# Kernel optimization log

Hardware: AMD Instinct MI355X
Metric: run time of the kernel (lower is better)

Reference implementation:

```python
import jax, jax.numpy as jnp
import numpy as np

N_NODES = 100000
N_EDGES = 3200000
F_IN = 128
F_HID = 16
F_OUT = 1


def setup_inputs() -> dict:
    key = jax.random.key(0)
    ks = jax.random.split(key, 8)
    x = jax.random.normal(ks[0], (N_NODES, F_IN), dtype=jnp.float32)
    src = jax.random.randint(ks[1], (N_EDGES,), 0, N_NODES, dtype=jnp.int32)
    dst = jax.random.randint(ks[2], (N_EDGES,), 0, N_NODES, dtype=jnp.int32)
    edge_w = jax.random.uniform(ks[3], (N_EDGES,), dtype=jnp.float32)
    W0 = jax.random.normal(ks[4], (F_IN, F_HID), dtype=jnp.float32) / np.sqrt(F_IN)
    b0 = jnp.zeros((F_HID,), dtype=jnp.float32)
    W1 = jax.random.normal(ks[5], (F_HID, F_OUT), dtype=jnp.float32) / np.sqrt(F_HID)
    b1 = jnp.zeros((F_OUT,), dtype=jnp.float32)
    return {"x": x, "src": src, "dst": dst, "edge_w": edge_w,
            "W0": W0, "b0": b0, "W1": W1, "b1": b1}


def _spmm(src, dst, edge_w, h):
    # sparse A (COO) @ dense h: gather rows at src, weight, scatter-add to dst
    msgs = h[src] * edge_w[:, None]            # [E, F]
    return jax.ops.segment_sum(msgs, dst, num_segments=N_NODES)  # [N, F]


def reference(x, src, dst, edge_w, W0, b0, W1, b1):
    # GCNConv layer 0: relu(A @ (x @ W0) + b0)
    z0 = x @ W0                                 # [N, 16] linear transform first
    h = jax.nn.relu(_spmm(src, dst, edge_w, z0) + b0)
    # (Dropout is identity at inference)
    # GCNConv layer 1: sigmoid(A @ (h @ W1) + b1)
    z1 = h @ W1                                 # [N, 1]
    out = jax.nn.sigmoid(_spmm(src, dst, edge_w, z1) + b1)
    return out
```

## Files before the change

### kernel.cpp

```cpp
#include <hip/hip_runtime.h>

#define N_NODES 100000
#define N_EDGES 3200000
#define F_IN 128
#define F_HID 16

#define BK_LG 9
#define BK_NODES 512
#define NBK ((N_NODES + BK_NODES - 1) / BK_NODES)
#define NBK_P 256
#define BCAP 17664
#define CH1 2048
#define NCH1 ((N_EDGES + CH1 - 1) / CH1)
#define CUR_STRIDE 16

__device__ __forceinline__ unsigned short f2bf_rne(float f) {
    unsigned u = __float_as_uint(f);
    u += 0x7FFFu + ((u >> 16) & 1u);
    return (unsigned short)(u >> 16);
}

__global__ __launch_bounds__(256) void k_pre(const float* __restrict__ x,
                                             const float* __restrict__ W0,
                                             unsigned short* __restrict__ z0b,
                                             const int* __restrict__ src,
                                             const int* __restrict__ dst,
                                             const float* __restrict__ ew,
                                             int* __restrict__ cursorC,
                                             int2* __restrict__ ebinC) {
    __shared__ __align__(16) char smem[24832];
    const int tid = threadIdx.x;

    if ((blockIdx.x & 1) == 0) {
        const int xb = blockIdx.x >> 1;
        unsigned short* xsb = (unsigned short*)smem;
        float* w0s = (float*)(smem + 16640);
        for (int i = tid; i < F_IN * F_HID; i += 256) w0s[i] = W0[i];
        const int row0 = xb * 64;
        for (int i = tid; i < 64 * 32; i += 256) {
            int r = i >> 5, c4 = i & 31;
            float4 v = make_float4(0.f, 0.f, 0.f, 0.f);
            int row = row0 + r;
            if (row < N_NODES) v = ((const float4*)(x + (size_t)row * F_IN))[c4];
            *(ushort2*)(xsb + r * 130 + c4 * 4)     = make_ushort2(f2bf_rne(v.x), f2bf_rne(v.y));
            *(ushort2*)(xsb + r * 130 + c4 * 4 + 2) = make_ushort2(f2bf_rne(v.z), f2bf_rne(v.w));
        }
        __syncthreads();
        const int r  = tid & 63;
        const int cg = tid >> 6;
        float a0 = 0.f, a1 = 0.f, a2 = 0.f, a3 = 0.f;
        #pragma unroll 4
        for (int k = 0; k < F_IN; k += 2) {
            unsigned u = *(const unsigned*)(xsb + r * 130 + k);
            float xv0 = __uint_as_float(u << 16);
            float xv1 = __uint_as_float(u & 0xFFFF0000u);
            const float* wr0 = w0s + k * F_HID + cg * 4;
            const float* wr1 = wr0 + F_HID;
            a0 = fmaf(xv0, wr0[0], a0); a1 = fmaf(xv0, wr0[1], a1);
            a2 = fmaf(xv0, wr0[2], a2); a3 = fmaf(xv0, wr0[3], a3);
            a0 = fmaf(xv1, wr1[0], a0); a1 = fmaf(xv1, wr1[1], a1);
            a2 = fmaf(xv1, wr1[2], a2); a3 = fmaf(xv1, wr1[3], a3);
        }
        int row = row0 + r;
        if (row < N_NODES) {
            ushort4 p = make_ushort4(f2bf_rne(a0), f2bf_rne(a1),
                                     f2bf_rne(a2), f2bf_rne(a3));
            *(ushort4*)(z0b + (size_t)row * F_HID + cg * 4) = p;
        }
    } else {
        const int ch = blockIdx.x >> 1;
        int2* stage = (int2*)smem;
        unsigned char* sbid = (unsigned char*)(smem + 16384);
        int* cnt  = (int*)(smem + 18432);
        int* excl = (int*)(smem + 19456);
        int* run  = (int*)(smem + 20480);
        int* gb   = (int*)(smem + 21504);
        int* alw  = (int*)(smem + 22528);
        int* wtot = (int*)(smem + 23552);
        const int e0  = ch * CH1;
        const int nch = min(CH1, N_EDGES - e0);

        cnt[tid] = 0;
        __syncthreads();

        int es[8], eb[8], edl[8]; float ww[8];
        #pragma unroll
        for (int k = 0; k < 8; ++k) {
            int idx = k * 256 + tid;
            if (idx < nch) {
                int e = e0 + idx;
                int d = dst[e];
                es[k]  = src[e];
                ww[k]  = ew[e];
                eb[k]  = d >> BK_LG;
                edl[k] = d & (BK_NODES - 1);
                atomicAdd(&cnt[eb[k]], 1);
            } else {
                eb[k] = -1;
            }
        }
        __syncthreads();

        {
            const int lane = tid & 63, wid = tid >> 6;
            int c_ = cnt[tid], inc = c_;
            #pragma unroll
            for (int off = 1; off < 64; off <<= 1) {
                int t = __shfl_up(inc, off);
                if (lane >= off) inc += t;
            }
            if (lane == 63) wtot[wid] = inc;
            __syncthreads();
            int base = 0;
            #pragma unroll
            for (int w = 0; w < 4; ++w) base += (w < wid) ? wtot[w] : 0;
            excl[tid] = base + inc - c_;
        }
        __syncthreads();

        if (tid < NBK) {
            int c = cnt[tid];
            if (c > 0) {
                int old = atomicAdd(&cursorC[tid * CUR_STRIDE], c);
                int a = BCAP - old;
                a = (a < 0) ? 0 : ((a > c) ? c : a);
                alw[tid] = a;
                gb[tid]  = tid * BCAP + old;
            } else {
                alw[tid] = 0;
                gb[tid]  = tid * BCAP;
            }
            run[tid] = 0;
        }
        __syncthreads();

        #pragma unroll
        for (int k = 0; k < 8; ++k) {
            if (eb[k] >= 0) {
                int b = eb[k];
                int p = excl[b] + atomicAdd(&run[b], 1);
                stage[p] = make_int2(__float_as_int(ww[k]), es[k] | (edl[k] << 17));
                sbid[p]  = (unsigned char)b;
            }
        }
        __syncthreads();

        for (int s = tid; s < nch; s += 256) {
            int b   = sbid[s];
            int off = s - excl[b];
            if (off < alw[b]) ebinC[(size_t)gb[b] + off] = stage[s];
        }
    }
}

__global__ __launch_bounds__(512) void k_sort2(const int* __restrict__ cursorC,
                                               const int2* __restrict__ ebinC,
                                               int2* __restrict__ sortedC,
                                               int2* __restrict__ rowinfo) {
    __shared__ int dcnt[BK_NODES], excl[BK_NODES], run[BK_NODES];
    __shared__ int wtot[8];
    const int tid = threadIdx.x, lane = tid & 63, wid = tid >> 6;
    const int c = blockIdx.x;
    dcnt[tid] = 0; run[tid] = 0;
    __syncthreads();
    const int   ecnt = min(cursorC[c * CUR_STRIDE], BCAP);
    const int2* eC   = ebinC + (size_t)c * BCAP;
    for (int i = tid; i < ecnt; i += 512) atomicAdd(&dcnt[eC[i].y >> 17], 1);
    __syncthreads();
    int d_ = dcnt[tid], inc = d_;
    #pragma unroll
    for (int off = 1; off < 64; off <<= 1) {
        int t = __shfl_up(inc, off);
        if (lane >= off) inc += t;
    }
    if (lane == 63) wtot[wid] = inc;
    __syncthreads();
    int base = 0;
    #pragma unroll
    for (int w = 0; w < 8; ++w) base += (w < wid) ? wtot[w] : 0;
    int ex = base + inc - d_;
    excl[tid] = ex;
    int v = c * BK_NODES + tid;
    if (v < N_NODES) rowinfo[v] = make_int2(c * BCAP + ex, d_);
    __syncthreads();
    int2* oB = sortedC + (size_t)c * BCAP;
    for (int i = tid; i < ecnt; i += 512) {
        int2 e = eC[i];
        int dl = e.y >> 17;
        int p  = excl[dl] + atomicAdd(&run[dl], 1);
        oB[p] = e;
    }
}

__global__ __launch_bounds__(256) void k_g0(const int2* __restrict__ rowinfo,
                                            const int2* __restrict__ sortedC,
                                            const unsigned short* __restrict__ z0b,
                                            const float* __restrict__ b0,
                                            const float* __restrict__ W1,
                                            float* __restrict__ z1) {
    __shared__ float b0s[16], w1s[16];
    const int tid = threadIdx.x;
    if (tid < 16) { b0s[tid] = b0[tid]; w1s[tid] = W1[tid]; }
    __syncthreads();
    const int lane = tid & 63;
    const int v    = blockIdx.x * 4 + (tid >> 6);
    if (v >= N_NODES) return;
    const int2 ri  = rowinfo[v];
    const int2* sl = sortedC + ri.x;
    const int dv   = ri.y;
    const int f2   = lane & 7;
    const int g    = lane >> 3;
    float acc0 = 0.f, acc1 = 0.f;
    for (int j = g; j < dv; j += 16) {
        int2 e0 = sl[j];
        int  j1 = j + 8;
        int2 e1 = (j1 < dv) ? sl[j1] : make_int2(0, 0);
        unsigned u0 = *(const unsigned*)(z0b + (size_t)(e0.y & 0x1FFFF) * F_HID + f2 * 2);
        unsigned u1 = *(const unsigned*)(z0b + (size_t)(e1.y & 0x1FFFF) * F_HID + f2 * 2);
        float w0 = __int_as_float(e0.x), w1 = __int_as_float(e1.x);
        acc0 = fmaf(__uint_as_float(u0 << 16),         w0, acc0);
        acc1 = fmaf(__uint_as_float(u0 & 0xFFFF0000u), w0, acc1);
        acc0 = fmaf(__uint_as_float(u1 << 16),         w1, acc0);
        acc1 = fmaf(__uint_as_float(u1 & 0xFFFF0000u), w1, acc1);
    }
    acc0 += __shfl_xor(acc0, 8);  acc1 += __shfl_xor(acc1, 8);
    acc0 += __shfl_xor(acc0, 16); acc1 += __shfl_xor(acc1, 16);
    acc0 += __shfl_xor(acc0, 32); acc1 += __shfl_xor(acc1, 32);
    float cc = fmaxf(acc0 + b0s[f2 * 2], 0.f) * w1s[f2 * 2]
             + fmaxf(acc1 + b0s[f2 * 2 + 1], 0.f) * w1s[f2 * 2 + 1];
    cc += __shfl_xor(cc, 1);
    cc += __shfl_xor(cc, 2);
    cc += __shfl_xor(cc, 4);
    if (lane == 0) z1[v] = cc;
}

__global__ __launch_bounds__(256) void k_g1(const int2* __restrict__ rowinfo,
                                            const int2* __restrict__ sortedC,
                                            const float* __restrict__ z1,
                                            const float* __restrict__ b1,
                                            float* __restrict__ out) {
    const int tid = threadIdx.x;
    const int l8  = tid & 7;
    const int v   = blockIdx.x * 32 + (tid >> 3);
    if (v >= N_NODES) return;
    const int2 ri  = rowinfo[v];
    const int2* sl = sortedC + ri.x;
    const int dv   = ri.y;
    float acc = 0.f;
    for (int j = l8; j < dv; j += 16) {
        int2 e0 = sl[j];
        int  j1 = j + 8;
        int2 e1 = (j1 < dv) ? sl[j1] : make_int2(0, 0);
        acc = fmaf(z1[e0.y & 0x1FFFF], __int_as_float(e0.x), acc);
        acc = fmaf(z1[e1.y & 0x1FFFF], __int_as_float(e1.x), acc);
    }
    #pragma unroll
    for (int off = 1; off < 8; off <<= 1) acc += __shfl_xor(acc, off);
    if (l8 == 0) {
        float t = acc + b1[0];
        out[v] = 1.f / (1.f + expf(-t));
    }
}

extern "C" void kernel_launch(void* const* d_in, const int* in_sizes, int n_in,
                              void* d_out, int out_size, void* d_ws, size_t ws_size,
                              hipStream_t stream) {
    const float* x   = (const float*)d_in[0];
    const int*   src = (const int*)d_in[1];
    const int*   dst = (const int*)d_in[2];
    const float* ew  = (const float*)d_in[3];
    const float* W0  = (const float*)d_in[4];
    const float* b0  = (const float*)d_in[5];
    const float* W1  = (const float*)d_in[6];
    const float* b1  = (const float*)d_in[7];
    float* out = (float*)d_out;

    unsigned short* z0b = (unsigned short*)d_ws;
    float* z1      = (float*)(z0b + (size_t)N_NODES * F_HID);
    int*   cursorC = (int*)(z1 + N_NODES);
    int2*  rowinfo = (int2*)(cursorC + NBK * CUR_STRIDE);
    int2*  ebinC   = rowinfo + N_NODES;
    int2*  sortedC = ebinC + (size_t)NBK * BCAP;

    hipMemsetAsync(cursorC, 0, (size_t)NBK * CUR_STRIDE * sizeof(int), stream);

    k_pre  <<<2 * NCH1, 256, 0, stream>>>(x, W0, z0b, src, dst, ew, cursorC, ebinC);
    k_sort2<<<NBK, 512, 0, stream>>>(cursorC, ebinC, sortedC, rowinfo);
    k_g0   <<<(N_NODES + 3) / 4,   256, 0, stream>>>(rowinfo, sortedC, z0b, b0, W1, z1);
    k_g1   <<<(N_NODES + 31) / 32, 256, 0, stream>>>(rowinfo, sortedC, z1, b1, out);
}
```

Baseline: 151.4 us.

## Restructure binning into coarse buckets and fuse fine sort with layer-0 gather

Edge binning now uses coarse 1024-node buckets in larger 4096-edge chunks, with per-wave histograms to cut shared atomic contention. A new fused kernel has each 128-node fine bucket scan its coarse slab, counting-sort its edges in LDS, write the sorted list for layer 1, and run the layer-0 gather directly from LDS. The x@W0 projection is split back into its own kernel, and the memset becomes a tiny kernel. The cost is that each coarse slab is read eight times, and there is less overlap between projection and binning.

```diff
diff --git a/kernel.cpp b/kernel.cpp
--- a/kernel.cpp
+++ b/kernel.cpp
@@ -5,13 +5,18 @@
 #define F_IN 128
 #define F_HID 16
 
-#define BK_LG 9
-#define BK_NODES 512
-#define NBK ((N_NODES + BK_NODES - 1) / BK_NODES)
-#define NBK_P 256
-#define BCAP 17664
-#define CH1 2048
-#define NCH1 ((N_EDGES + CH1 - 1) / CH1)
+#define BK_LG 7
+#define BK_NODES 128
+#define NB ((N_NODES + BK_NODES - 1) / BK_NODES)
+#define BCAPF 4736
+#define CLG 10
+#define CNODES 1024
+#define NBC ((N_NODES + CNODES - 1) / CNODES)
+#define NBC_P 128
+#define BCAPC 34816
+#define CHUNK1 4096
+#define NCH1 ((N_EDGES + CHUNK1 - 1) / CHUNK1)
+#define NXB ((N_NODES + 63) / 64)
 #define CUR_STRIDE 16
 
 __device__ __forceinline__ unsigned short f2bf_rne(float f) {
@@ -20,222 +25,258 @@
     return (unsigned short)(u >> 16);
 }
 
-__global__ __launch_bounds__(256) void k_pre(const float* __restrict__ x,
+__global__ __launch_bounds__(256) void k_zc(int* __restrict__ cursorC) {
+    int i = blockIdx.x * 256 + threadIdx.x;
+    if (i < NBC * CUR_STRIDE) cursorC[i] = 0;
+}
+
+__global__ __launch_bounds__(512) void k_bin1(const int* __restrict__ src,
+                                              const int* __restrict__ dst,
+                                              const float* __restrict__ ew,
+                                              int* __restrict__ cursorC,
+                                              int2* __restrict__ ebinC) {
+    __shared__ int2 stage[CHUNK1];
+    __shared__ unsigned char sbid[CHUNK1];
+    __shared__ int cntw[8 * NBC_P];
+    __shared__ int runw[8 * NBC_P];
+    __shared__ int basew[8 * NBC_P];
+    __shared__ int cnt[NBC_P], excl[NBC_P], gb[NBC_P], alw[NBC_P];
+    __shared__ int wtot[2];
+    const int tid  = threadIdx.x;
+    const int lane = tid & 63, wid = tid >> 6;
+    const int e0   = blockIdx.x * CHUNK1;
+    const int nch  = min(CHUNK1, N_EDGES - e0);
+
+    for (int i = tid; i < 8 * NBC_P; i += 512) { cntw[i] = 0; runw[i] = 0; }
+    __syncthreads();
+
+    int es[8], eb[8], edl[8]; float ww[8];
+    #pragma unroll
+    for (int k = 0; k < 8; ++k) {
+        int idx = k * 512 + tid;
+        if (idx < nch) {
+            int e = e0 + idx;
+            int d = dst[e];
+            es[k]  = src[e];
+            ww[k]  = ew[e];
+            eb[k]  = d >> CLG;
+            edl[k] = d & (CNODES - 1);
+            atomicAdd(&cntw[wid * NBC_P + eb[k]], 1);
+        } else {
+            eb[k] = -1;
+        }
+    }
+    __syncthreads();
+
+    if (tid < NBC_P) {
+        int t = 0;
+        #pragma unroll
+        for (int w = 0; w < 8; ++w) t += cntw[w * NBC_P + tid];
+        cnt[tid] = t;
+    }
+    __syncthreads();
+
+    int inc = 0, c_ = 0;
+    if (tid < NBC_P) {
+        c_ = cnt[tid];
+        inc = c_;
+        #pragma unroll
+        for (int off = 1; off < 64; off <<= 1) {
+            int t = __shfl_up(inc, off);
+            if (lane >= off) inc += t;
+        }
+        if (lane == 63) wtot[tid >> 6] = inc;
+    }
+    __syncthreads();
+    if (tid < NBC_P) {
+        int base = (tid >= 64) ? wtot[0] : 0;
+        excl[tid] = base + inc - c_;
+    }
+    if (tid < NBC) {
+        int c = cnt[tid];
+        if (c > 0) {
+            int old = atomicAdd(&cursorC[tid * CUR_STRIDE], c);
+            int a = BCAPC - old;
+            a = (a < 0) ? 0 : ((a > c) ? c : a);
+            alw[tid] = a;
+            gb[tid]  = tid * BCAPC + old;
+        } else {
+            alw[tid] = 0;
+            gb[tid]  = tid * BCAPC;
+        }
+    }
+    __syncthreads();
+
+    if (tid < NBC_P) {
+        int bb = excl[tid];
+        #pragma unroll
+        for (int w = 0; w < 8; ++w) { basew[w * NBC_P + tid] = bb; bb += cntw[w * NBC_P + tid]; }
+    }
+    __syncthreads();
+
+    #pragma unroll
+    for (int k = 0; k < 8; ++k) {
+        if (eb[k] >= 0) {
+            int b = eb[k];
+            int p = basew[wid * NBC_P + b] + atomicAdd(&runw[wid * NBC_P + b], 1);
+            stage[p] = make_int2(__float_as_int(ww[k]), es[k] | (edl[k] << 17));
+            sbid[p]  = (unsigned char)b;
+        }
+    }
+    __syncthreads();
+
+    for (int s = tid; s < nch; s += 512) {
+        int b   = sbid[s];
+        int off = s - excl[b];
+        if (off < alw[b]) ebinC[(size_t)gb[b] + off] = stage[s];
+    }
+}
+
+__global__ __launch_bounds__(256) void k_xw0(const float* __restrict__ x,
                                              const float* __restrict__ W0,
-                                             unsigned short* __restrict__ z0b,
-                                             const int* __restrict__ src,
-                                             const int* __restrict__ dst,
-                                             const float* __restrict__ ew,
-                                             int* __restrict__ cursorC,
-                                             int2* __restrict__ ebinC) {
-    __shared__ __align__(16) char smem[24832];
+                                             unsigned short* __restrict__ z0b) {
+    __shared__ unsigned short xsb[64 * 130];
+    __shared__ float w0s[F_IN * F_HID];
     const int tid = threadIdx.x;
-
-    if ((blockIdx.x & 1) == 0) {
-        const int xb = blockIdx.x >> 1;
-        unsigned short* xsb = (unsigned short*)smem;
-        float* w0s = (float*)(smem + 16640);
-        for (int i = tid; i < F_IN * F_HID; i += 256) w0s[i] = W0[i];
-        const int row0 = xb * 64;
-        for (int i = tid; i < 64 * 32; i += 256) {
-            int r = i >> 5, c4 = i & 31;
-            float4 v = make_float4(0.f, 0.f, 0.f, 0.f);
-            int row = row0 + r;
-            if (row < N_NODES) v = ((const float4*)(x + (size_t)row * F_IN))[c4];
-            *(ushort2*)(xsb + r * 130 + c4 * 4)     = make_ushort2(f2bf_rne(v.x), f2bf_rne(v.y));
-            *(ushort2*)(xsb + r * 130 + c4 * 4 + 2) = make_ushort2(f2bf_rne(v.z), f2bf_rne(v.w));
-        }
-        __syncthreads();
-        const int r  = tid & 63;
-        const int cg = tid >> 6;
-        float a0 = 0.f, a1 = 0.f, a2 = 0.f, a3 = 0.f;
-        #pragma unroll 4
-        for (int k = 0; k < F_IN; k += 2) {
-            unsigned u = *(const unsigned*)(xsb + r * 130 + k);
-            float xv0 = __uint_as_float(u << 16);
-            float xv1 = __uint_as_float(u & 0xFFFF0000u);
-            const float* wr0 = w0s + k * F_HID + cg * 4;
-            const float* wr1 = wr0 + F_HID;
-            a0 = fmaf(xv0, wr0[0], a0); a1 = fmaf(xv0, wr0[1], a1);
-            a2 = fmaf(xv0, wr0[2], a2); a3 = fmaf(xv0, wr0[3], a3);
-            a0 = fmaf(xv1, wr1[0], a0); a1 = fmaf(xv1, wr1[1], a1);
-            a2 = fmaf(xv1, wr1[2], a2); a3 = fmaf(xv1, wr1[3], a3);
-        }
+    for (int i = tid; i < F_IN * F_HID; i += 256) w0s[i] = W0[i];
+    const int row0 = blockIdx.x * 64;
+    for (int i = tid; i < 64 * 32; i += 256) {
+        int r = i >> 5, c4 = i & 31;
+        float4 v = make_float4(0.f, 0.f, 0.f, 0.f);
         int row = row0 + r;
-        if (row < N_NODES) {
-            ushort4 p = make_ushort4(f2bf_rne(a0), f2bf_rne(a1),
-                                     f2bf_rne(a2), f2bf_rne(a3));
-            *(ushort4*)(z0b + (size_t)row * F_HID + cg * 4) = p;
-        }
-    } else {
-        const int ch = blockIdx.x >> 1;
-        int2* stage = (int2*)smem;
-        unsigned char* sbid = (unsigned char*)(smem + 16384);
-        int* cnt  = (int*)(smem + 18432);
-        int* excl = (int*)(smem + 19456);
-        int* run  = (int*)(smem + 20480);
-        int* gb   = (int*)(smem + 21504);
-        int* alw  = (int*)(smem + 22528);
-        int* wtot = (int*)(smem + 23552);
-        const int e0  = ch * CH1;
-        const int nch = min(CH1, N_EDGES - e0);
-
-        cnt[tid] = 0;
-        __syncthreads();
-
-        int es[8], eb[8], edl[8]; float ww[8];
+        if (row < N_NODES) v = ((const float4*)(x + (size_t)row * F_IN))[c4];
+        *(ushort2*)(xsb + r * 130 + c4 * 4)     = make_ushort2(f2bf_rne(v.x), f2bf_rne(v.y));
+        *(ushort2*)(xsb + r * 130 + c4 * 4 + 2) = make_ushort2(f2bf_rne(v.z), f2bf_rne(v.w));
+    }
+    __syncthreads();
+    const int r  = tid & 63;
+    const int cg = tid >> 6;
+    float a0 = 0.f, a1 = 0.f, a2 = 0.f, a3 = 0.f;
+    #pragma unroll 4
+    for (int k = 0; k < F_IN; k += 2) {
+        unsigned u = *(const unsigned*)(xsb + r * 130 + k);
+        float xv0 = __uint_as_float(u << 16);
+        float xv1 = __uint_as_float(u & 0xFFFF0000u);
+        const float* wr0 = w0s + k * F_HID + cg * 4;
+        const float* wr1 = wr0 + F_HID;
+        a0 = fmaf(xv0, wr0[0], a0); a1 = fmaf(xv0, wr0[1], a1);
+        a2 = fmaf(xv0, wr0[2], a2); a3 = fmaf(xv0, wr0[3], a3);
+        a0 = fmaf(xv1, wr1[0], a0); a1 = fmaf(xv1, wr1[1], a1);
+        a2 = fmaf(xv1, wr1[2], a2); a3 = fmaf(xv1, wr1[3], a3);
+    }
+    int row = row0 + r;
+    if (row < N_NODES) {
+        ushort4 p = make_ushort4(f2bf_rne(a0), f2bf_rne(a1),
+                                 f2bf_rne(a2), f2bf_rne(a3));
+        *(ushort4*)(z0b + (size_t)row * F_HID + cg * 4) = p;
+    }
+}
+
+__global__ __launch_bounds__(512) void k_sg0(const int* __restrict__ cursorC,
+                                             const int2* __restrict__ ebinC,
+                                             const unsigned short* __restrict__ z0b,
+                                             const float* __restrict__ b0,
+                                             const float* __restrict__ W1,
+                                             float* __restrict__ z1,
+                                             int2* __restrict__ sortedF,
+                                             int2* __restrict__ rowinfo) {
+    __shared__ int2 sorted[BCAPF];
+    __shared__ int hist[BK_NODES], scn[BK_NODES], run[BK_NODES];
+    __shared__ int wtot[2];
+    __shared__ float b0s[16], w1s[16];
+    const int tid  = threadIdx.x;
+    const int lane = tid & 63, wid = tid >> 6;
+    const int fb   = blockIdx.x;
+    if (fb >= NB) return;
+    const int c = fb >> 3, f = fb & 7;
+    if (tid < 16)       { b0s[tid] = b0[tid]; w1s[tid] = W1[tid]; }
+    if (tid < BK_NODES) { hist[tid] = 0; run[tid] = 0; }
+    __syncthreads();
+
+    const int   ecnt = min(cursorC[c * CUR_STRIDE], BCAPC);
+    const int2* slab = ebinC + (size_t)c * BCAPC;
+
+    for (int i = tid; i < ecnt; i += 512) {
+        int dlc = slab[i].y >> 17;
+        if ((dlc >> BK_LG) == f) atomicAdd(&hist[dlc & (BK_NODES - 1)], 1);
+    }
+    __syncthreads();
+
+    int inc = 0, d_ = 0;
+    if (tid < BK_NODES) {
+        d_ = hist[tid];
+        inc = d_;
         #pragma unroll
-        for (int k = 0; k < 8; ++k) {
-            int idx = k * 256 + tid;
-            if (idx < nch) {
-                int e = e0 + idx;
-                int d = dst[e];
-                es[k]  = src[e];
-                ww[k]  = ew[e];
-                eb[k]  = d >> BK_LG;
-                edl[k] = d & (BK_NODES - 1);
-                atomicAdd(&cnt[eb[k]], 1);
-            } else {
-                eb[k] = -1;
-            }
-        }
-        __syncthreads();
-
-        {
-            const int lane = tid & 63, wid = tid >> 6;
-            int c_ = cnt[tid], inc = c_;
-            #pragma unroll
-            for (int off = 1; off < 64; off <<= 1) {
-                int t = __shfl_up(inc, off);
-                if (lane >= off) inc += t;
-            }
-            if (lane == 63) wtot[wid] = inc;
-            __syncthreads();
-            int base = 0;
-            #pragma unroll
-            for (int w = 0; w < 4; ++w) base += (w < wid) ? wtot[w] : 0;
-            excl[tid] = base + inc - c_;
-        }
-        __syncthreads();
-
-        if (tid < NBK) {
-            int c = cnt[tid];
-            if (c > 0) {
-                int old = atomicAdd(&cursorC[tid * CUR_STRIDE], c);
-                int a = BCAP - old;
-                a = (a < 0) ? 0 : ((a > c) ? c : a);
-                alw[tid] = a;
-                gb[tid]  = tid * BCAP + old;
-            } else {
-                alw[tid] = 0;
-                gb[tid]  = tid * BCAP;
-            }
-            run[tid] = 0;
-        }
-        __syncthreads();
-
-        #pragma unroll
-        for (int k = 0; k < 8; ++k) {
-            if (eb[k] >= 0) {
-                int b = eb[k];
-                int p = excl[b] + atomicAdd(&run[b], 1);
-                stage[p] = make_int2(__float_as_int(ww[k]), es[k] | (edl[k] << 17));
-                sbid[p]  = (unsigned char)b;
-            }
-        }
-        __syncthreads();
-
-        for (int s = tid; s < nch; s += 256) {
-            int b   = sbid[s];
-            int off = s - excl[b];
-            if (off < alw[b]) ebinC[(size_t)gb[b] + off] = stage[s];
-        }
-    }
-}
-
-__global__ __launch_bounds__(512) void k_sort2(const int* __restrict__ cursorC,
-                                               const int2* __restrict__ ebinC,
-                                               int2* __restrict__ sortedC,
-                                               int2* __restrict__ rowinfo) {
-    __shared__ int dcnt[BK_NODES], excl[BK_NODES], run[BK_NODES];
-    __shared__ int wtot[8];
-    const int tid = threadIdx.x, lane = tid & 63, wid = tid >> 6;
-    const int c = blockIdx.x;
-    dcnt[tid] = 0; run[tid] = 0;
-    __syncthreads();
-    const int   ecnt = min(cursorC[c * CUR_STRIDE], BCAP);
-    const int2* eC   = ebinC + (size_t)c * BCAP;
-    for (int i = tid; i < ecnt; i += 512) atomicAdd(&dcnt[eC[i].y >> 17], 1);
-    __syncthreads();
-    int d_ = dcnt[tid], inc = d_;
-    #pragma unroll
-    for (int off = 1; off < 64; off <<= 1) {
-        int t = __shfl_up(inc, off);
-        if (lane >= off) inc += t;
-    }
-    if (lane == 63) wtot[wid] = inc;
-    __syncthreads();
-    int base = 0;
-    #pragma unroll
-    for (int w = 0; w < 8; ++w) base += (w < wid) ? wtot[w] : 0;
-    int ex = base + inc - d_;
-    excl[tid] = ex;
-    int v = c * BK_NODES + tid;
-    if (v < N_NODES) rowinfo[v] = make_int2(c * BCAP + ex, d_);
-    __syncthreads();
-    int2* oB = sortedC + (size_t)c * BCAP;
+        for (int off = 1; off < 64; off <<= 1) {
+            int t = __shfl_up(inc, off);
+            if (lane >= off) inc += t;
+        }
+        if (lane == 63) wtot[tid >> 6] = inc;
+    }
+    __syncthreads();
+    if (tid < BK_NODES) {
+        int base = (tid >= 64) ? wtot[0] : 0;
+        scn[tid] = base + inc - d_;
+    }
+    __syncthreads();
+
     for (int i = tid; i < ecnt; i += 512) {
-        int2 e = eC[i];
-        int dl = e.y >> 17;
-        int p  = excl[dl] + atomicAdd(&run[dl], 1);
-        oB[p] = e;
-    }
-}
-
-__global__ __launch_bounds__(256) void k_g0(const int2* __restrict__ rowinfo,
-                                            const int2* __restrict__ sortedC,
-                                            const unsigned short* __restrict__ z0b,
-                                            const float* __restrict__ b0,
-                                            const float* __restrict__ W1,
-                                            float* __restrict__ z1) {
-    __shared__ float b0s[16], w1s[16];
-    const int tid = threadIdx.x;
-    if (tid < 16) { b0s[tid] = b0[tid]; w1s[tid] = W1[tid]; }
-    __syncthreads();
-    const int lane = tid & 63;
-    const int v    = blockIdx.x * 4 + (tid >> 6);
-    if (v >= N_NODES) return;
-    const int2 ri  = rowinfo[v];
-    const int2* sl = sortedC + ri.x;
-    const int dv   = ri.y;
-    const int f2   = lane & 7;
-    const int g    = lane >> 3;
-    float acc0 = 0.f, acc1 = 0.f;
-    for (int j = g; j < dv; j += 16) {
-        int2 e0 = sl[j];
-        int  j1 = j + 8;
-        int2 e1 = (j1 < dv) ? sl[j1] : make_int2(0, 0);
-        unsigned u0 = *(const unsigned*)(z0b + (size_t)(e0.y & 0x1FFFF) * F_HID + f2 * 2);
-        unsigned u1 = *(const unsigned*)(z0b + (size_t)(e1.y & 0x1FFFF) * F_HID + f2 * 2);
-        float w0 = __int_as_float(e0.x), w1 = __int_as_float(e1.x);
-        acc0 = fmaf(__uint_as_float(u0 << 16),         w0, acc0);
-        acc1 = fmaf(__uint_as_float(u0 & 0xFFFF0000u), w0, acc1);
-        acc0 = fmaf(__uint_as_float(u1 << 16),         w1, acc0);
-        acc1 = fmaf(__uint_as_float(u1 & 0xFFFF0000u), w1, acc1);
-    }
-    acc0 += __shfl_xor(acc0, 8);  acc1 += __shfl_xor(acc1, 8);
-    acc0 += __shfl_xor(acc0, 16); acc1 += __shfl_xor(acc1, 16);
-    acc0 += __shfl_xor(acc0, 32); acc1 += __shfl_xor(acc1, 32);
-    float cc = fmaxf(acc0 + b0s[f2 * 2], 0.f) * w1s[f2 * 2]
-             + fmaxf(acc1 + b0s[f2 * 2 + 1], 0.f) * w1s[f2 * 2 + 1];
-    cc += __shfl_xor(cc, 1);
-    cc += __shfl_xor(cc, 2);
-    cc += __shfl_xor(cc, 4);
-    if (lane == 0) z1[v] = cc;
+        int2 e  = slab[i];
+        int dlc = e.y >> 17;
+        if ((dlc >> BK_LG) == f) {
+            int dl = dlc & (BK_NODES - 1);
+            int p  = scn[dl] + atomicAdd(&run[dl], 1);
+            if (p < BCAPF) sorted[p] = make_int2(e.x, (e.y & 0x1FFFF) | (dl << 17));
+        }
+    }
+    __syncthreads();
+
+    const int fcnt = min(scn[BK_NODES - 1] + hist[BK_NODES - 1], BCAPF);
+    int2* oB = sortedF + (size_t)fb * BCAPF;
+    for (int s = tid; s < fcnt; s += 512) oB[s] = sorted[s];
+    if (tid < BK_NODES) {
+        int v = fb * BK_NODES + tid;
+        if (v < N_NODES) {
+            int beg = min(scn[tid], BCAPF);
+            int dv  = min(hist[tid], BCAPF - beg);
+            rowinfo[v] = make_int2(fb * BCAPF + beg, dv);
+        }
+    }
+
+    for (int n = wid; n < BK_NODES; n += 8) {
+        const int v = fb * BK_NODES + n;
+        if (v >= N_NODES) continue;
+        const int beg = min(scn[n], BCAPF);
+        const int dv  = min(hist[n], BCAPF - beg);
+        const int f2  = lane & 7;
+        const int g   = lane >> 3;
+        float acc0 = 0.f, acc1 = 0.f;
+        for (int j = g; j < dv; j += 16) {
+            int2 e0 = sorted[beg + j];
+            int  j1 = j + 8;
+            int2 e1 = (j1 < dv) ? sorted[beg + j1] : make_int2(0, 0);
+            unsigned u0 = *(const unsigned*)(z0b + (size_t)(e0.y & 0x1FFFF) * F_HID + f2 * 2);
+            unsigned u1 = *(const unsigned*)(z0b + (size_t)(e1.y & 0x1FFFF) * F_HID + f2 * 2);
+            float w0 = __int_as_float(e0.x), w1 = __int_as_float(e1.x);
+            acc0 = fmaf(__uint_as_float(u0 << 16),         w0, acc0);
+            acc1 = fmaf(__uint_as_float(u0 & 0xFFFF0000u), w0, acc1);
+            acc0 = fmaf(__uint_as_float(u1 << 16),         w1, acc0);
+            acc1 = fmaf(__uint_as_float(u1 & 0xFFFF0000u), w1, acc1);
+        }
+        acc0 += __shfl_xor(acc0, 8);  acc1 += __shfl_xor(acc1, 8);
+        acc0 += __shfl_xor(acc0, 16); acc1 += __shfl_xor(acc1, 16);
+        acc0 += __shfl_xor(acc0, 32); acc1 += __shfl_xor(acc1, 32);
+        float cc = fmaxf(acc0 + b0s[f2 * 2], 0.f) * w1s[f2 * 2]
+                 + fmaxf(acc1 + b0s[f2 * 2 + 1], 0.f) * w1s[f2 * 2 + 1];
+        cc += __shfl_xor(cc, 1);
+        cc += __shfl_xor(cc, 2);
+        cc += __shfl_xor(cc, 4);
+        if (lane == 0) z1[v] = cc;
+    }
 }
 
 __global__ __launch_bounds__(256) void k_g1(const int2* __restrict__ rowinfo,
-                                            const int2* __restrict__ sortedC,
+                                            const int2* __restrict__ sortedF,
                                             const float* __restrict__ z1,
                                             const float* __restrict__ b1,
                                             float* __restrict__ out) {
@@ -244,7 +285,7 @@
     const int v   = blockIdx.x * 32 + (tid >> 3);
     if (v >= N_NODES) return;
     const int2 ri  = rowinfo[v];
-    const int2* sl = sortedC + ri.x;
+    const int2* sl = sortedF + ri.x;
     const int dv   = ri.y;
     float acc = 0.f;
     for (int j = l8; j < dv; j += 16) {
@@ -278,14 +319,14 @@
     unsigned short* z0b = (unsigned short*)d_ws;
     float* z1      = (float*)(z0b + (size_t)N_NODES * F_HID);
     int*   cursorC = (int*)(z1 + N_NODES);
-    int2*  rowinfo = (int2*)(cursorC + NBK * CUR_STRIDE);
+    int2*  rowinfo = (int2*)(cursorC + NBC * CUR_STRIDE);
     int2*  ebinC   = rowinfo + N_NODES;
-    int2*  sortedC = ebinC + (size_t)NBK * BCAP;
-
-    hipMemsetAsync(cursorC, 0, (size_t)NBK * CUR_STRIDE * sizeof(int), stream);
-
-    k_pre  <<<2 * NCH1, 256, 0, stream>>>(x, W0, z0b, src, dst, ew, cursorC, ebinC);
-    k_sort2<<<NBK, 512, 0, stream>>>(cursorC, ebinC, sortedC, rowinfo);
-    k_g0   <<<(N_NODES + 3) / 4,   256, 0, stream>>>(rowinfo, sortedC, z0b, b0, W1, z1);
-    k_g1   <<<(N_NODES + 31) / 32, 256, 0, stream>>>(rowinfo, sortedC, z1, b1, out);
-}
+    int2*  sortedF = ebinC + (size_t)NBC * BCAPC;
+
+    k_zc  <<<(NBC * CUR_STRIDE + 255) / 256, 256, 0, stream>>>(cursorC);
+    k_bin1<<<NCH1, 512, 0, stream>>>(src, dst, ew, cursorC, ebinC);
+    k_xw0 <<<NXB, 256, 0, stream>>>(x, W0, z0b);
+    k_sg0 <<<NB, 512, 0, stream>>>(cursorC, ebinC, z0b, b0, W1, z1,
+                                   sortedF, rowinfo);
+    k_g1  <<<(N_NODES + 31) / 32, 256, 0, stream>>>(rowinfo, sortedF, z1, b1, out);
+}
```

Result: slower. 164.9 us (+8.9%).
